# Performance work log

Measured on AMD Instinct MI355X. Metric: run time of the kernel, lower is better.

Reference implementation:

```python
import jax, jax.numpy as jnp
import numpy as np

N_NODES = 20000
N_EDGES = 640000


def graph_conv(x, src, dst, W, b, n_nodes):
    """DGL GraphConv with norm='both': D_in^{-1/2} A D_out^{-1/2} X W + b."""
    ones = jnp.ones(src.shape[0], dtype=x.dtype)
    deg_out = jnp.maximum(jax.ops.segment_sum(ones, src, num_segments=n_nodes), 1.0)
    deg_in = jnp.maximum(jax.ops.segment_sum(ones, dst, num_segments=n_nodes), 1.0)
    xs = x * (deg_out ** -0.5)[:, None]          # scale src features
    agg = jax.ops.segment_sum(xs[src], dst, num_segments=n_nodes)  # [N, d]
    agg = agg * (deg_in ** -0.5)[:, None]
    return agg @ W + b


def setup_inputs() -> dict:
    key = jax.random.key(0)
    ks = jax.random.split(key, 10)
    d = 256
    scale = 1.0 / np.sqrt(d)
    return {
        "x": jax.random.normal(ks[0], (N_NODES, d), dtype=jnp.float32),
        "side_src": jax.random.randint(ks[1], (N_EDGES,), 0, N_NODES),
        "side_dst": jax.random.randint(ks[2], (N_EDGES,), 0, N_NODES),
        "upd_src": jax.random.randint(ks[3], (N_EDGES,), 0, N_NODES),
        "upd_dst": jax.random.randint(ks[4], (N_EDGES,), 0, N_NODES),
        "W1_side": jax.random.normal(ks[5], (d, d), dtype=jnp.float32) * scale,
        "b1_side": jnp.zeros((d,), dtype=jnp.float32),
        "W1_upd": jax.random.normal(ks[6], (d, d), dtype=jnp.float32) * scale,
        "b1_upd": jnp.zeros((d,), dtype=jnp.float32),
        "W2_side": jax.random.normal(ks[7], (d, d), dtype=jnp.float32) * scale,
        "b2_side": jnp.zeros((d,), dtype=jnp.float32),
        "W2_upd": jax.random.normal(ks[8], (d, d), dtype=jnp.float32) * scale,
        "b2_upd": jnp.zeros((d,), dtype=jnp.float32),
    }


def reference(x, side_src, side_dst, upd_src, upd_dst,
              W1_side, b1_side, W1_upd, b1_upd,
              W2_side, b2_side, W2_upd, b2_upd):
    n = x.shape[0]
    # layer 1: HeteroGraphConv with aggregate='sum' over relations, then relu
    h = (graph_conv(x, side_src, side_dst, W1_side, b1_side, n)
         + graph_conv(x, upd_src, upd_dst, W1_upd, b1_upd, n))
    h = jax.nn.relu(h)
    # layer 2
    out = (graph_conv(h, side_src, side_dst, W2_side, b2_side, n)
           + graph_conv(h, upd_src, upd_dst, W2_upd, b2_upd, n))
    return out
```

## Files before the change

### kernel.cpp

```cpp
#include <hip/hip_runtime.h>

typedef __attribute__((ext_vector_type(8))) short short8;
typedef __attribute__((ext_vector_type(4))) float f32x4;

#define SCHUNK 2048
#define MAXN   20480
#define NSLICE 8
#define NPB    80

__device__ inline unsigned short f2bf(float v) {
    unsigned u = __float_as_uint(v);
    u += 0x7FFFu + ((u >> 16) & 1u);
    return (unsigned short)(u >> 16);
}
__device__ inline float bf2f(unsigned short h) {
    return __uint_as_float((unsigned)h << 16);
}

__global__ void bias_sum_kernel(const float* __restrict__ b1s, const float* __restrict__ b1u,
                                const float* __restrict__ b2s, const float* __restrict__ b2u,
                                float* __restrict__ bsum1, float* __restrict__ bsum2) {
    int i = threadIdx.x;
    bsum1[i] = b1s[i] + b1u[i];
    bsum2[i] = b2s[i] + b2u[i];
}

__global__ void wprep_kernel(const float* __restrict__ W1s, const float* __restrict__ W1u,
                             const float* __restrict__ W2s, const float* __restrict__ W2u,
                             unsigned short* __restrict__ Bpk1, unsigned short* __restrict__ Bpk2) {
    int k = blockIdx.x;
    int nn = threadIdx.x;
    int layer = blockIdx.y;
    const float* Ws = layer ? W2s : W1s;
    const float* Wu = layer ? W2u : W1u;
    float w = (k < 256) ? Ws[k * 256 + nn] : Wu[(k - 256) * 256 + nn];
    unsigned short hi = f2bf(w);
    unsigned short lo = f2bf(w - bf2f(hi));
    unsigned short* B = layer ? Bpk2 : Bpk1;
    size_t frag = ((size_t)(nn >> 4) * 16 + (k >> 5)) * 2;
    size_t addr = frag * 512 + ((nn & 15) + ((k >> 3) & 3) * 16) * 8 + (k & 7);
    B[addr] = hi;
    B[addr + 512] = lo;
}

__global__ __launch_bounds__(256) void hist_kernel(
    const int* __restrict__ sS, const int* __restrict__ dS,
    const int* __restrict__ sU, const int* __restrict__ dU,
    int Es, int Eu, int n, int nblk, unsigned int* __restrict__ histG) {
    __shared__ unsigned int h[MAXN];
    const int rel = blockIdx.y;
    const int* src = rel ? sU : sS;
    const int* dst = rel ? dU : dS;
    int E = rel ? Eu : Es;
    int b = blockIdx.x;
    int chunk = (E + nblk - 1) / nblk;
    int beg = b * chunk;
    int end = min(E, beg + chunk);
    for (int i = threadIdx.x; i < n; i += 256) h[i] = 0u;
    __syncthreads();
    for (int i = beg + threadIdx.x; i < end; i += 256) {
        atomicAdd(&h[src[i]], 1u);
        atomicAdd(&h[dst[i]], 0x10000u);
    }
    __syncthreads();
    unsigned int* out = histG + ((size_t)rel * nblk + b) * n;
    for (int i = threadIdx.x; i < n; i += 256) out[i] = h[i];
}

__global__ void totals_kernel(const unsigned int* __restrict__ histG, int n, int nblk,
                              float* __restrict__ sOutS, float* __restrict__ sInS,
                              float* __restrict__ sOutU, float* __restrict__ sInU,
                              int* __restrict__ degInS, int* __restrict__ degInU) {
    const int rel = blockIdx.y;
    int i = blockIdx.x * 256 + threadIdx.x;
    if (i >= n) return;
    const unsigned int* hg = histG + (size_t)rel * nblk * n;
    unsigned int lo = 0, hi = 0;
    for (int b = 0; b < nblk; ++b) {
        unsigned int v = hg[(size_t)b * n + i];
        lo += v & 0xFFFFu;
        hi += v >> 16;
    }
    float so = rsqrtf((float)(lo > 1u ? lo : 1u));
    float si = rsqrtf((float)(hi > 1u ? hi : 1u));
    if (rel) { sOutU[i] = so; sInU[i] = si; degInU[i] = (int)hi; }
    else     { sOutS[i] = so; sInS[i] = si; degInS[i] = (int)hi; }
}

__global__ __launch_bounds__(256) void scan_part_kernel(const int* __restrict__ degA,
                                                        const int* __restrict__ degB,
                                                        int n, int NB, int* __restrict__ bsum) {
    const int rel = blockIdx.y;
    const int* deg = rel ? degB : degA;
    int t = threadIdx.x;
    int base = blockIdx.x * SCHUNK + t * 8;
    int s = 0;
    if (base + 8 <= n) {
        int4 a = *(const int4*)(deg + base);
        int4 b = *(const int4*)(deg + base + 4);
        s = a.x + a.y + a.z + a.w + b.x + b.y + b.z + b.w;
    } else {
        for (int i = 0; i < 8; ++i)
            if (base + i < n) s += deg[base + i];
    }
    __shared__ int sm[256];
    sm[t] = s;
    __syncthreads();
    for (int off = 128; off > 0; off >>= 1) {
        if (t < off) sm[t] += sm[t + off];
        __syncthreads();
    }
    if (t == 0) bsum[rel * NB + blockIdx.x] = sm[0];
}

__global__ void scan_mid_kernel(int* __restrict__ bsum, int NB,
                                int* __restrict__ rpA, int* __restrict__ rpB, int n) {
    int t = threadIdx.x;
    if (t >= 2) return;
    int* bs = bsum + t * NB;
    int run = 0;
    for (int i = 0; i < NB; ++i) {
        int v = bs[i];
        bs[i] = run;
        run += v;
    }
    int* rp = t ? rpB : rpA;
    rp[n] = run;
}

__global__ __launch_bounds__(256) void scan_final_kernel(const int* __restrict__ degA,
                                                         const int* __restrict__ degB,
                                                         const int* __restrict__ bsum,
                                                         int n, int NB,
                                                         int* __restrict__ rpA,
                                                         int* __restrict__ rpB) {
    const int rel = blockIdx.y;
    const int* deg = rel ? degB : degA;
    int* rp = rel ? rpB : rpA;
    int t = threadIdx.x;
    int base = blockIdx.x * SCHUNK + t * 8;
    int v[8];
    if (base + 8 <= n) {
        int4 a = *(const int4*)(deg + base);
        int4 b = *(const int4*)(deg + base + 4);
        v[0] = a.x; v[1] = a.y; v[2] = a.z; v[3] = a.w;
        v[4] = b.x; v[5] = b.y; v[6] = b.z; v[7] = b.w;
    } else {
        for (int i = 0; i < 8; ++i) v[i] = (base + i < n) ? deg[base + i] : 0;
    }
    int s = 0;
    #pragma unroll
    for (int i = 0; i < 8; ++i) s += v[i];
    __shared__ int sm[256];
    sm[t] = s;
    __syncthreads();
    #pragma unroll
    for (int off = 1; off < 256; off <<= 1) {
        int y = (t >= off) ? sm[t - off] : 0;
        __syncthreads();
        sm[t] += y;
        __syncthreads();
    }
    int run = bsum[rel * NB + blockIdx.x] + sm[t] - s;
    #pragma unroll
    for (int i = 0; i < 8; ++i) {
        if (base + i < n) rp[base + i] = run;
        run += v[i];
    }
}

__global__ void offsets_kernel(const unsigned int* __restrict__ histG,
                               const int* __restrict__ rpS, const int* __restrict__ rpU,
                               int n, int nblk, int* __restrict__ offsG) {
    const int rel = blockIdx.y;
    int i = blockIdx.x * 256 + threadIdx.x;
    if (i >= n) return;
    const unsigned int* hg = histG + (size_t)rel * nblk * n;
    int* og = offsG + (size_t)rel * nblk * n;
    int run = (rel ? rpU : rpS)[i];
    for (int b = 0; b < nblk; ++b) {
        og[(size_t)b * n + i] = run;
        run += (int)(hg[(size_t)b * n + i] >> 16);
    }
}

__global__ __launch_bounds__(256) void csr_scatter_kernel(
    const int* __restrict__ sS, const int* __restrict__ dS,
    const int* __restrict__ sU, const int* __restrict__ dU,
    int Es, int Eu, int n, int nblk, const int* __restrict__ offsG,
    const float* __restrict__ sOutS, const float* __restrict__ sOutU,
    int2* __restrict__ csrPS, int2* __restrict__ csrPU) {
    __shared__ int off[MAXN];
    const int rel = blockIdx.y;
    const int* src = rel ? sU : sS;
    const int* dst = rel ? dU : dS;
    const float* so = rel ? sOutU : sOutS;
    int2* csrP = rel ? csrPU : csrPS;
    int E = rel ? Eu : Es;
    int b = blockIdx.x;
    int chunk = (E + nblk - 1) / nblk;
    int beg = b * chunk;
    int end = min(E, beg + chunk);
    const int* og = offsG + ((size_t)rel * nblk + b) * n;
    for (int i = threadIdx.x; i < n; i += 256) off[i] = og[i];
    __syncthreads();
    for (int i = beg + threadIdx.x; i < end; i += 256) {
        int s = src[i];
        int pos = atomicAdd(&off[dst[i]], 1);
        csrP[pos] = make_int2(s, __float_as_int(so[s]));
    }
}

__global__ __launch_bounds__(256) void pull_slice_kernel(
    const float4* __restrict__ xin,
    const int2* __restrict__ csrPS, const int2* __restrict__ csrPU,
    const int* __restrict__ rpS, const int* __restrict__ rpU,
    const float* __restrict__ sinS, const float* __restrict__ sinU,
    unsigned short* __restrict__ aggPk, int n) {
    int bid = blockIdx.x;
    int slice = bid & (NSLICE - 1);
    int rest = bid >> 3;
    int rel = rest & 1;
    int chunk = rest >> 1;
    const int2* csrP = rel ? csrPU : csrPS;
    const int* rp = rel ? rpU : rpS;
    const float* sinv = rel ? sinU : sinS;

    int wave = threadIdx.x >> 6;
    int lane = threadIdx.x & 63;
    int sub = lane >> 3;
    int sl = lane & 7;
    int fbase = slice * 8 + sl;

    int start = chunk * NPB;
    int lim = min(n, start + NPB);
    for (int node = start + wave; node < lim; node += 4) {
        int beg = rp[node], end = rp[node + 1];
        float ax = 0.f, ay = 0.f, az = 0.f, aw = 0.f;
        for (int eb = beg; eb < end; eb += 64) {
            int cnt = end - eb;
            if (cnt > 64) cnt = 64;
            int myu = 0;
            float myw = 0.f;
            if (lane < cnt) {
                int2 p = csrP[eb + lane];
                myu = p.x;
                myw = __int_as_float(p.y);
            }
            int jmax = (cnt + 7) >> 3;
            int j = 0;
            for (; j + 4 <= jmax; j += 4) {
                int i0 = j * 8 + sub;
                int u0 = __shfl(myu, i0);
                int u1 = __shfl(myu, i0 + 8);
                int u2 = __shfl(myu, i0 + 16);
                int u3 = __shfl(myu, i0 + 24);
                float w0 = __shfl(myw, i0);
                float w1 = __shfl(myw, i0 + 8);
                float w2 = __shfl(myw, i0 + 16);
                float w3 = __shfl(myw, i0 + 24);
                float4 a0 = xin[(size_t)u0 * 64 + fbase];
                float4 a1 = xin[(size_t)u1 * 64 + fbase];
                float4 a2 = xin[(size_t)u2 * 64 + fbase];
                float4 a3 = xin[(size_t)u3 * 64 + fbase];
                ax += w0 * a0.x + w1 * a1.x + w2 * a2.x + w3 * a3.x;
                ay += w0 * a0.y + w1 * a1.y + w2 * a2.y + w3 * a3.y;
                az += w0 * a0.z + w1 * a1.z + w2 * a2.z + w3 * a3.z;
                aw += w0 * a0.w + w1 * a1.w + w2 * a2.w + w3 * a3.w;
            }
            for (; j < jmax; ++j) {
                int idx = j * 8 + sub;
                int u = __shfl(myu, idx);
                float w = __shfl(myw, idx);
                float4 a = xin[(size_t)u * 64 + fbase];
                ax += w * a.x; ay += w * a.y; az += w * a.z; aw += w * a.w;
            }
        }
        ax += __shfl_xor(ax, 8);  ax += __shfl_xor(ax, 16); ax += __shfl_xor(ax, 32);
        ay += __shfl_xor(ay, 8);  ay += __shfl_xor(ay, 16); ay += __shfl_xor(ay, 32);
        az += __shfl_xor(az, 8);  az += __shfl_xor(az, 16); az += __shfl_xor(az, 32);
        aw += __shfl_xor(aw, 8);  aw += __shfl_xor(aw, 16); aw += __shfl_xor(aw, 32);
        if (sub == 0) {
            float si = sinv[node];
            float vx = si * ax, vy = si * ay, vz = si * az, vw = si * aw;
            ushort4 hi4 = make_ushort4(f2bf(vx), f2bf(vy), f2bf(vz), f2bf(vw));
            ushort4 lo4 = make_ushort4(f2bf(vx - bf2f(hi4.x)), f2bf(vy - bf2f(hi4.y)),
                                       f2bf(vz - bf2f(hi4.z)), f2bf(vw - bf2f(hi4.w)));
            int kstepg = rel * 8 + slice;
            size_t frag = ((size_t)(node >> 4) * 16 + kstepg) * 2;
            size_t addr = frag * 512 + ((node & 15) + (sl >> 1) * 16) * 8 + (sl & 1) * 4;
            *(ushort4*)&aggPk[addr] = hi4;
            *(ushort4*)&aggPk[addr + 512] = lo4;
        }
    }
}

#define GLOAD(AH, AL, BH, BL, KS) {                                          \
    _Pragma("unroll")                                                        \
    for (int fr = 0; fr < 2; ++fr) {                                         \
        size_t fa = ((size_t)(mt0 + fr) * 16 + (KS)) * 128 + lane;           \
        AH[fr] = Apk[fa];                                                    \
        AL[fr] = Apk[fa + 64];                                               \
    }                                                                        \
    _Pragma("unroll")                                                        \
    for (int fc = 0; fc < 4; ++fc) {                                         \
        size_t fb = ((size_t)(nt0 + fc) * 16 + (KS)) * 128 + lane;           \
        BH[fc] = Bpk[fb];                                                    \
        BL[fc] = Bpk[fb + 64];                                               \
    }                                                                        \
}

#define GMFMA(AH, AL, BH, BL) {                                              \
    _Pragma("unroll")                                                        \
    for (int fr = 0; fr < 2; ++fr)                                           \
    _Pragma("unroll")                                                        \
    for (int fc = 0; fc < 4; ++fc) {                                         \
        acc[fr][fc] = __builtin_amdgcn_mfma_f32_16x16x32_bf16(AH[fr], BH[fc], acc[fr][fc], 0, 0, 0); \
        acc[fr][fc] = __builtin_amdgcn_mfma_f32_16x16x32_bf16(AL[fr], BH[fc], acc[fr][fc], 0, 0, 0); \
        acc[fr][fc] = __builtin_amdgcn_mfma_f32_16x16x32_bf16(AH[fr], BL[fc], acc[fr][fc], 0, 0, 0); \
    }                                                                        \
}

template <int RELU>
__global__ __launch_bounds__(256) void gemm_mfma_kernel(
    const short8* __restrict__ Apk, const short8* __restrict__ Bpk,
    const float* __restrict__ bias, float* __restrict__ C, int M) {
    int lane = threadIdx.x & 63;
    int wv = threadIdx.x >> 6;
    int m0 = blockIdx.x * 32;
    if (m0 >= M) return;
    int mt0 = blockIdx.x * 2;
    int nt0 = wv * 4;
    int col0 = wv * 64;
    int frow = lane & 15;

    f32x4 acc[2][4];
    #pragma unroll
    for (int fr = 0; fr < 2; ++fr)
        #pragma unroll
        for (int fc = 0; fc < 4; ++fc)
            acc[fr][fc] = (f32x4){0.f, 0.f, 0.f, 0.f};

    short8 ahA[2], alA[2], bhA[4], blA[4];
    short8 ahB[2], alB[2], bhB[4], blB[4];
    GLOAD(ahA, alA, bhA, blA, 0);
    #pragma unroll
    for (int kp = 0; kp < 8; ++kp) {
        GLOAD(ahB, alB, bhB, blB, 2 * kp + 1);
        GMFMA(ahA, alA, bhA, blA);
        if (kp < 7) GLOAD(ahA, alA, bhA, blA, 2 * kp + 2);
        GMFMA(ahB, alB, bhB, blB);
    }

    #pragma unroll
    for (int fr = 0; fr < 2; ++fr)
        #pragma unroll
        for (int fc = 0; fc < 4; ++fc) {
            int c = col0 + fc * 16 + frow;
            float bc = bias[c];
            int rb = m0 + fr * 16 + (lane >> 4) * 4;
            #pragma unroll
            for (int j = 0; j < 4; ++j) {
                int r = rb + j;
                if (r < M) {
                    float v = acc[fr][fc][j] + bc;
                    if (RELU) v = fmaxf(v, 0.f);
                    C[(size_t)r * 256 + c] = v;
                }
            }
        }
}

extern "C" void kernel_launch(void* const* d_in, const int* in_sizes, int n_in,
                              void* d_out, int out_size, void* d_ws, size_t ws_size,
                              hipStream_t stream) {
    const float* x   = (const float*)d_in[0];
    const int* sS    = (const int*)d_in[1];
    const int* dS    = (const int*)d_in[2];
    const int* sU    = (const int*)d_in[3];
    const int* dU    = (const int*)d_in[4];
    const float* W1s = (const float*)d_in[5];
    const float* b1s = (const float*)d_in[6];
    const float* W1u = (const float*)d_in[7];
    const float* b1u = (const float*)d_in[8];
    const float* W2s = (const float*)d_in[9];
    const float* b2s = (const float*)d_in[10];
    const float* W2u = (const float*)d_in[11];
    const float* b2u = (const float*)d_in[12];
    float* out = (float*)d_out;

    const int n  = in_sizes[0] / 256;
    const int Es = in_sizes[1];
    const int Eu = in_sizes[3];
    const int NB = (n + SCHUNK - 1) / SCHUNK;
    const int mtiles = (n + 15) / 16;
    const size_t BPK_BYTES = (size_t)16 * 16 * 2 * 512 * 2;

    auto plan = [&](int nb) -> size_t {
        size_t t = 0;
        auto add = [&](size_t b) { t = (t + 255) & ~(size_t)255; t += b; };
        add((size_t)2 * nb * n * 4);
        add((size_t)2 * nb * n * 4);
        add((size_t)(n + 1) * 4); add((size_t)(n + 1) * 4);
        add((size_t)n * 4); add((size_t)n * 4); add((size_t)n * 4); add((size_t)n * 4);
        add((size_t)n * 4); add((size_t)n * 4);
        add(256 * 4); add(256 * 4);
        add((size_t)2 * NB * 4);
        add((size_t)Es * 8); add((size_t)Eu * 8);
        add(2 * BPK_BYTES);
        add((size_t)mtiles * 16 * 2 * 512 * 2);
        add((size_t)n * 256 * 4);
        return t;
    };
    const int nblk = (plan(128) <= ws_size) ? 128 : 32;

    char* ws = (char*)d_ws;
    size_t off = 0;
    auto alloc = [&](size_t bytes) -> void* {
        off = (off + 255) & ~(size_t)255;
        void* p = ws + off;
        off += bytes;
        return p;
    };

    unsigned int* histG = (unsigned int*)alloc((size_t)2 * nblk * n * 4);
    int* offsG   = (int*)alloc((size_t)2 * nblk * n * 4);
    int* rpS     = (int*)alloc((size_t)(n + 1) * 4);
    int* rpU     = (int*)alloc((size_t)(n + 1) * 4);
    float* sOutS = (float*)alloc((size_t)n * 4);
    float* sInS  = (float*)alloc((size_t)n * 4);
    float* sOutU = (float*)alloc((size_t)n * 4);
    float* sInU  = (float*)alloc((size_t)n * 4);
    int* degInS  = (int*)alloc((size_t)n * 4);
    int* degInU  = (int*)alloc((size_t)n * 4);
    float* bsum1 = (float*)alloc(256 * 4);
    float* bsum2 = (float*)alloc(256 * 4);
    int* bsumBlk = (int*)alloc((size_t)2 * NB * 4);
    int2* csrPS  = (int2*)alloc((size_t)Es * 8);
    int2* csrPU  = (int2*)alloc((size_t)Eu * 8);
    unsigned short* Bpk1 = (unsigned short*)alloc(2 * BPK_BYTES);
    unsigned short* Bpk2 = Bpk1 + BPK_BYTES / 2;
    unsigned short* aggPk = (unsigned short*)alloc((size_t)mtiles * 16 * 2 * 512 * 2);
    float* h     = (float*)alloc((size_t)n * 256 * 4);

    bias_sum_kernel<<<1, 256, 0, stream>>>(b1s, b1u, b2s, b2u, bsum1, bsum2);
    wprep_kernel<<<dim3(512, 2), 256, 0, stream>>>(W1s, W1u, W2s, W2u, Bpk1, Bpk2);
    dim3 hg(nblk, 2);
    hist_kernel<<<hg, 256, 0, stream>>>(sS, dS, sU, dU, Es, Eu, n, nblk, histG);
    dim3 tg((n + 255) / 256, 2);
    totals_kernel<<<tg, 256, 0, stream>>>(histG, n, nblk, sOutS, sInS, sOutU, sInU,
                                          degInS, degInU);
    dim3 sg(NB, 2);
    scan_part_kernel<<<sg, 256, 0, stream>>>(degInS, degInU, n, NB, bsumBlk);
    scan_mid_kernel<<<1, 64, 0, stream>>>(bsumBlk, NB, rpS, rpU, n);
    scan_final_kernel<<<sg, 256, 0, stream>>>(degInS, degInU, bsumBlk, n, NB, rpS, rpU);
    offsets_kernel<<<tg, 256, 0, stream>>>(histG, rpS, rpU, n, nblk, offsG);
    csr_scatter_kernel<<<hg, 256, 0, stream>>>(sS, dS, sU, dU, Es, Eu, n, nblk, offsG,
                                               sOutS, sOutU, csrPS, csrPU);

    int chunks = (n + NPB - 1) / NPB;
    int pullGrid = NSLICE * 2 * chunks;
    int gemmGrid = (n + 31) / 32;
    const float4* x4 = (const float4*)x;
    const float4* h4 = (const float4*)h;
    const short8* A8 = (const short8*)aggPk;
    const short8* B81 = (const short8*)Bpk1;
    const short8* B82 = (const short8*)Bpk2;

    pull_slice_kernel<<<pullGrid, 256, 0, stream>>>(x4, csrPS, csrPU, rpS, rpU,
                                                    sInS, sInU, aggPk, n);
    gemm_mfma_kernel<1><<<gemmGrid, 256, 0, stream>>>(A8, B81, bsum1, h, n);
    pull_slice_kernel<<<pullGrid, 256, 0, stream>>>(h4, csrPS, csrPU, rpS, rpU,
                                                    sInS, sInU, aggPk, n);
    gemm_mfma_kernel<0><<<gemmGrid, 256, 0, stream>>>(A8, B82, bsum2, out, n);
}
```

Baseline: 487.7 us.

## Degree-sort nodes so each 8-lane group pulls its own node, retile GEMM

Adds a counting-sort kernel that orders destination nodes by in-degree. The pull kernel now assigns one node to each 8-lane subgroup instead of one node per wave, and sorting balances trip counts so neighboring subgroups do similar work. This removes the cross-lane reductions and the idle lanes on low-degree nodes. The GEMM is retiled to 80-row blocks with 512 threads and loses its double-buffered loads, and NPB changes to 64. The extra sort kernel runs on only two blocks, and because nodes are permuted, aggPk writes are scattered.

```diff
diff --git a/kernel.cpp b/kernel.cpp
--- a/kernel.cpp
+++ b/kernel.cpp
@@ -6,7 +6,7 @@
 #define SCHUNK 2048
 #define MAXN   20480
 #define NSLICE 8
-#define NPB    80
+#define NPB    64
 
 __device__ inline unsigned short f2bf(float v) {
     unsigned u = __float_as_uint(v);
@@ -87,6 +87,40 @@
     else     { sOutS[i] = so; sInS[i] = si; degInS[i] = (int)hi; }
 }
 
+__global__ __launch_bounds__(256) void sortperm_kernel(
+    const int* __restrict__ degInS, const int* __restrict__ degInU,
+    int n, int* __restrict__ permS, int* __restrict__ permU) {
+    const int rel = blockIdx.x;
+    const int* deg = rel ? degInU : degInS;
+    int* perm = rel ? permU : permS;
+    __shared__ unsigned cnt[256];
+    __shared__ unsigned scan[256];
+    int t = threadIdx.x;
+    cnt[t] = 0;
+    __syncthreads();
+    for (int i = t; i < n; i += 256) {
+        int b = deg[i]; b = b > 255 ? 255 : b;
+        atomicAdd(&cnt[b], 1u);
+    }
+    __syncthreads();
+    unsigned v = cnt[t];
+    scan[t] = v;
+    __syncthreads();
+    for (int off = 1; off < 256; off <<= 1) {
+        unsigned y = (t >= off) ? scan[t - off] : 0u;
+        __syncthreads();
+        scan[t] += y;
+        __syncthreads();
+    }
+    cnt[t] = scan[t] - v;
+    __syncthreads();
+    for (int i = t; i < n; i += 256) {
+        int b = deg[i]; b = b > 255 ? 255 : b;
+        unsigned pos = atomicAdd(&cnt[b], 1u);
+        perm[pos] = i;
+    }
+}
+
 __global__ __launch_bounds__(256) void scan_part_kernel(const int* __restrict__ degA,
                                                         const int* __restrict__ degB,
                                                         int n, int NB, int* __restrict__ bsum) {
@@ -216,6 +250,7 @@
     const int2* __restrict__ csrPS, const int2* __restrict__ csrPU,
     const int* __restrict__ rpS, const int* __restrict__ rpU,
     const float* __restrict__ sinS, const float* __restrict__ sinU,
+    const int* __restrict__ permS, const int* __restrict__ permU,
     unsigned short* __restrict__ aggPk, int n) {
     int bid = blockIdx.x;
     int slice = bid & (NSLICE - 1);
@@ -225,68 +260,45 @@
     const int2* csrP = rel ? csrPU : csrPS;
     const int* rp = rel ? rpU : rpS;
     const float* sinv = rel ? sinU : sinS;
+    const int* perm = rel ? permU : permS;
 
     int wave = threadIdx.x >> 6;
     int lane = threadIdx.x & 63;
     int sub = lane >> 3;
     int sl = lane & 7;
     int fbase = slice * 8 + sl;
+    int subbase = lane & 56;
+    int kstepg = rel * 8 + slice;
 
     int start = chunk * NPB;
     int lim = min(n, start + NPB);
-    for (int node = start + wave; node < lim; node += 4) {
-        int beg = rp[node], end = rp[node + 1];
+    for (int nb = start + wave * 8; nb < lim; nb += 32) {
+        int pidx = nb + sub;
+        bool valid = pidx < lim;
+        int node = valid ? perm[pidx] : 0;
+        int beg = 0, end = 0;
+        if (valid) { beg = rp[node]; end = rp[node + 1]; }
         float ax = 0.f, ay = 0.f, az = 0.f, aw = 0.f;
-        for (int eb = beg; eb < end; eb += 64) {
-            int cnt = end - eb;
-            if (cnt > 64) cnt = 64;
-            int myu = 0;
-            float myw = 0.f;
-            if (lane < cnt) {
-                int2 p = csrP[eb + lane];
-                myu = p.x;
-                myw = __int_as_float(p.y);
-            }
-            int jmax = (cnt + 7) >> 3;
-            int j = 0;
-            for (; j + 4 <= jmax; j += 4) {
-                int i0 = j * 8 + sub;
-                int u0 = __shfl(myu, i0);
-                int u1 = __shfl(myu, i0 + 8);
-                int u2 = __shfl(myu, i0 + 16);
-                int u3 = __shfl(myu, i0 + 24);
-                float w0 = __shfl(myw, i0);
-                float w1 = __shfl(myw, i0 + 8);
-                float w2 = __shfl(myw, i0 + 16);
-                float w3 = __shfl(myw, i0 + 24);
-                float4 a0 = xin[(size_t)u0 * 64 + fbase];
-                float4 a1 = xin[(size_t)u1 * 64 + fbase];
-                float4 a2 = xin[(size_t)u2 * 64 + fbase];
-                float4 a3 = xin[(size_t)u3 * 64 + fbase];
-                ax += w0 * a0.x + w1 * a1.x + w2 * a2.x + w3 * a3.x;
-                ay += w0 * a0.y + w1 * a1.y + w2 * a2.y + w3 * a3.y;
-                az += w0 * a0.z + w1 * a1.z + w2 * a2.z + w3 * a3.z;
-                aw += w0 * a0.w + w1 * a1.w + w2 * a2.w + w3 * a3.w;
-            }
-            for (; j < jmax; ++j) {
-                int idx = j * 8 + sub;
-                int u = __shfl(myu, idx);
-                float w = __shfl(myw, idx);
+        int eb = beg;
+        while (__any(eb < end)) {
+            int ei = eb + sl;
+            int2 p = make_int2(0, 0);
+            if (ei < end) p = csrP[ei];
+            #pragma unroll
+            for (int j = 0; j < 8; ++j) {
+                int u = __shfl(p.x, subbase | j);
+                float w = __int_as_float(__shfl(p.y, subbase | j));
                 float4 a = xin[(size_t)u * 64 + fbase];
                 ax += w * a.x; ay += w * a.y; az += w * a.z; aw += w * a.w;
             }
+            eb += 8;
         }
-        ax += __shfl_xor(ax, 8);  ax += __shfl_xor(ax, 16); ax += __shfl_xor(ax, 32);
-        ay += __shfl_xor(ay, 8);  ay += __shfl_xor(ay, 16); ay += __shfl_xor(ay, 32);
-        az += __shfl_xor(az, 8);  az += __shfl_xor(az, 16); az += __shfl_xor(az, 32);
-        aw += __shfl_xor(aw, 8);  aw += __shfl_xor(aw, 16); aw += __shfl_xor(aw, 32);
-        if (sub == 0) {
+        if (valid) {
             float si = sinv[node];
             float vx = si * ax, vy = si * ay, vz = si * az, vw = si * aw;
             ushort4 hi4 = make_ushort4(f2bf(vx), f2bf(vy), f2bf(vz), f2bf(vw));
             ushort4 lo4 = make_ushort4(f2bf(vx - bf2f(hi4.x)), f2bf(vy - bf2f(hi4.y)),
                                        f2bf(vz - bf2f(hi4.z)), f2bf(vw - bf2f(hi4.w)));
-            int kstepg = rel * 8 + slice;
             size_t frag = ((size_t)(node >> 4) * 16 + kstepg) * 2;
             size_t addr = frag * 512 + ((node & 15) + (sl >> 1) * 16) * 8 + (sl & 1) * 4;
             *(ushort4*)&aggPk[addr] = hi4;
@@ -295,67 +307,55 @@
     }
 }
 
-#define GLOAD(AH, AL, BH, BL, KS) {                                          \
-    _Pragma("unroll")                                                        \
-    for (int fr = 0; fr < 2; ++fr) {                                         \
-        size_t fa = ((size_t)(mt0 + fr) * 16 + (KS)) * 128 + lane;           \
-        AH[fr] = Apk[fa];                                                    \
-        AL[fr] = Apk[fa + 64];                                               \
-    }                                                                        \
-    _Pragma("unroll")                                                        \
-    for (int fc = 0; fc < 4; ++fc) {                                         \
-        size_t fb = ((size_t)(nt0 + fc) * 16 + (KS)) * 128 + lane;           \
-        BH[fc] = Bpk[fb];                                                    \
-        BL[fc] = Bpk[fb + 64];                                               \
-    }                                                                        \
-}
-
-#define GMFMA(AH, AL, BH, BL) {                                              \
-    _Pragma("unroll")                                                        \
-    for (int fr = 0; fr < 2; ++fr)                                           \
-    _Pragma("unroll")                                                        \
-    for (int fc = 0; fc < 4; ++fc) {                                         \
-        acc[fr][fc] = __builtin_amdgcn_mfma_f32_16x16x32_bf16(AH[fr], BH[fc], acc[fr][fc], 0, 0, 0); \
-        acc[fr][fc] = __builtin_amdgcn_mfma_f32_16x16x32_bf16(AL[fr], BH[fc], acc[fr][fc], 0, 0, 0); \
-        acc[fr][fc] = __builtin_amdgcn_mfma_f32_16x16x32_bf16(AH[fr], BL[fc], acc[fr][fc], 0, 0, 0); \
-    }                                                                        \
-}
-
 template <int RELU>
-__global__ __launch_bounds__(256) void gemm_mfma_kernel(
+__global__ __launch_bounds__(512) void gemm_mfma_kernel(
     const short8* __restrict__ Apk, const short8* __restrict__ Bpk,
     const float* __restrict__ bias, float* __restrict__ C, int M) {
     int lane = threadIdx.x & 63;
     int wv = threadIdx.x >> 6;
-    int m0 = blockIdx.x * 32;
+    int mt0 = blockIdx.x * 5;
+    int m0 = blockIdx.x * 80;
     if (m0 >= M) return;
-    int mt0 = blockIdx.x * 2;
-    int nt0 = wv * 4;
-    int col0 = wv * 64;
+    int nt0 = wv * 2;
+    int col0 = wv * 32;
     int frow = lane & 15;
 
-    f32x4 acc[2][4];
-    #pragma unroll
-    for (int fr = 0; fr < 2; ++fr)
+    f32x4 acc[5][2];
+    #pragma unroll
+    for (int fr = 0; fr < 5; ++fr)
         #pragma unroll
-        for (int fc = 0; fc < 4; ++fc)
+        for (int fc = 0; fc < 2; ++fc)
             acc[fr][fc] = (f32x4){0.f, 0.f, 0.f, 0.f};
 
-    short8 ahA[2], alA[2], bhA[4], blA[4];
-    short8 ahB[2], alB[2], bhB[4], blB[4];
-    GLOAD(ahA, alA, bhA, blA, 0);
-    #pragma unroll
-    for (int kp = 0; kp < 8; ++kp) {
-        GLOAD(ahB, alB, bhB, blB, 2 * kp + 1);
-        GMFMA(ahA, alA, bhA, blA);
-        if (kp < 7) GLOAD(ahA, alA, bhA, blA, 2 * kp + 2);
-        GMFMA(ahB, alB, bhB, blB);
-    }
-
-    #pragma unroll
-    for (int fr = 0; fr < 2; ++fr)
+    #pragma unroll
+    for (int ks = 0; ks < 16; ++ks) {
+        short8 ah[5], al[5], bh[2], bl[2];
         #pragma unroll
-        for (int fc = 0; fc < 4; ++fc) {
+        for (int fr = 0; fr < 5; ++fr) {
+            size_t fa = ((size_t)(mt0 + fr) * 16 + ks) * 128 + lane;
+            ah[fr] = Apk[fa];
+            al[fr] = Apk[fa + 64];
+        }
+        #pragma unroll
+        for (int fc = 0; fc < 2; ++fc) {
+            size_t fb = ((size_t)(nt0 + fc) * 16 + ks) * 128 + lane;
+            bh[fc] = Bpk[fb];
+            bl[fc] = Bpk[fb + 64];
+        }
+        #pragma unroll
+        for (int fr = 0; fr < 5; ++fr)
+            #pragma unroll
+            for (int fc = 0; fc < 2; ++fc) {
+                acc[fr][fc] = __builtin_amdgcn_mfma_f32_16x16x32_bf16(ah[fr], bh[fc], acc[fr][fc], 0, 0, 0);
+                acc[fr][fc] = __builtin_amdgcn_mfma_f32_16x16x32_bf16(al[fr], bh[fc], acc[fr][fc], 0, 0, 0);
+                acc[fr][fc] = __builtin_amdgcn_mfma_f32_16x16x32_bf16(ah[fr], bl[fc], acc[fr][fc], 0, 0, 0);
+            }
+    }
+
+    #pragma unroll
+    for (int fr = 0; fr < 5; ++fr)
+        #pragma unroll
+        for (int fc = 0; fc < 2; ++fc) {
             int c = col0 + fc * 16 + frow;
             float bc = bias[c];
             int rb = m0 + fr * 16 + (lane >> 4) * 4;
@@ -393,7 +393,8 @@
     const int Es = in_sizes[1];
     const int Eu = in_sizes[3];
     const int NB = (n + SCHUNK - 1) / SCHUNK;
-    const int mtiles = (n + 15) / 16;
+    const int gemmGrid = (n + 79) / 80;
+    const size_t AGG_BYTES = (size_t)gemmGrid * 5 * 16 * 2 * 512 * 2;
     const size_t BPK_BYTES = (size_t)16 * 16 * 2 * 512 * 2;
 
     auto plan = [&](int nb) -> size_t {
@@ -404,11 +405,12 @@
         add((size_t)(n + 1) * 4); add((size_t)(n + 1) * 4);
         add((size_t)n * 4); add((size_t)n * 4); add((size_t)n * 4); add((size_t)n * 4);
         add((size_t)n * 4); add((size_t)n * 4);
+        add((size_t)n * 4); add((size_t)n * 4);
         add(256 * 4); add(256 * 4);
         add((size_t)2 * NB * 4);
         add((size_t)Es * 8); add((size_t)Eu * 8);
         add(2 * BPK_BYTES);
-        add((size_t)mtiles * 16 * 2 * 512 * 2);
+        add(AGG_BYTES);
         add((size_t)n * 256 * 4);
         return t;
     };
@@ -433,6 +435,8 @@
     float* sInU  = (float*)alloc((size_t)n * 4);
     int* degInS  = (int*)alloc((size_t)n * 4);
     int* degInU  = (int*)alloc((size_t)n * 4);
+    int* permS   = (int*)alloc((size_t)n * 4);
+    int* permU   = (int*)alloc((size_t)n * 4);
     float* bsum1 = (float*)alloc(256 * 4);
     float* bsum2 = (float*)alloc(256 * 4);
     int* bsumBlk = (int*)alloc((size_t)2 * NB * 4);
@@ -440,7 +444,7 @@
     int2* csrPU  = (int2*)alloc((size_t)Eu * 8);
     unsigned short* Bpk1 = (unsigned short*)alloc(2 * BPK_BYTES);
     unsigned short* Bpk2 = Bpk1 + BPK_BYTES / 2;
-    unsigned short* aggPk = (unsigned short*)alloc((size_t)mtiles * 16 * 2 * 512 * 2);
+    unsigned short* aggPk = (unsigned short*)alloc(AGG_BYTES);
     float* h     = (float*)alloc((size_t)n * 256 * 4);
 
     bias_sum_kernel<<<1, 256, 0, stream>>>(b1s, b1u, b2s, b2u, bsum1, bsum2);
@@ -450,6 +454,7 @@
     dim3 tg((n + 255) / 256, 2);
     totals_kernel<<<tg, 256, 0, stream>>>(histG, n, nblk, sOutS, sInS, sOutU, sInU,
                                           degInS, degInU);
+    sortperm_kernel<<<2, 256, 0, stream>>>(degInS, degInU, n, permS, permU);
     dim3 sg(NB, 2);
     scan_part_kernel<<<sg, 256, 0, stream>>>(degInS, degInU, n, NB, bsumBlk);
     scan_mid_kernel<<<1, 64, 0, stream>>>(bsumBlk, NB, rpS, rpU, n);
@@ -460,7 +465,6 @@
 
     int chunks = (n + NPB - 1) / NPB;
     int pullGrid = NSLICE * 2 * chunks;
-    int gemmGrid = (n + 31) / 32;
     const float4* x4 = (const float4*)x;
     const float4* h4 = (const float4*)h;
     const short8* A8 = (const short8*)aggPk;
@@ -468,9 +472,9 @@
     const short8* B82 = (const short8*)Bpk2;
 
     pull_slice_kernel<<<pullGrid, 256, 0, stream>>>(x4, csrPS, csrPU, rpS, rpU,
-                                                    sInS, sInU, aggPk, n);
-    gemm_mfma_kernel<1><<<gemmGrid, 256, 0, stream>>>(A8, B81, bsum1, h, n);
+                                                    sInS, sInU, permS, permU, aggPk, n);
+    gemm_mfma_kernel<1><<<gemmGrid, 512, 0, stream>>>(A8, B81, bsum1, h, n);
     pull_slice_kernel<<<pullGrid, 256, 0, stream>>>(h4, csrPS, csrPU, rpS, rpU,
-                                                    sInS, sInU, aggPk, n);
-    gemm_mfma_kernel<0><<<gemmGrid, 256, 0, stream>>>(A8, B82, bsum2, out, n);
-}
+                                                    sInS, sInU, permS, permU, aggPk, n);
+    gemm_mfma_kernel<0><<<gemmGrid, 512, 0, stream>>>(A8, B82, bsum2, out, n);
+}
```

New measurement: 550.7 us. 12.9% more time.

## Retile MFMA GEMM to 80-row blocks with 8 waves and halve pull chunk

Applied to the files above, without the earlier changes.

The GEMM now uses 512-thread blocks. Each block covers 80 rows (5 m-tiles) and each wave covers 32 columns, replacing 32-row blocks of 4 waves with 64 columns each. The explicit double-buffered register prefetch is dropped in favour of a simple per-k-step load then MFMA loop. The aggregate buffer is padded to a multiple of 80 rows, and the pull kernel's nodes per block drop from 80 to 40 to launch more blocks. The aim is more reuse of each loaded A fragment across waves and better parallelism, at the risk of exposed load latency without the prefetch and a different occupancy profile.

```diff
diff --git a/kernel.cpp b/kernel.cpp
--- a/kernel.cpp
+++ b/kernel.cpp
@@ -6,7 +6,7 @@
 #define SCHUNK 2048
 #define MAXN   20480
 #define NSLICE 8
-#define NPB    80
+#define NPB    40
 
 __device__ inline unsigned short f2bf(float v) {
     unsigned u = __float_as_uint(v);
@@ -231,6 +231,7 @@
     int sub = lane >> 3;
     int sl = lane & 7;
     int fbase = slice * 8 + sl;
+    int kstepg = rel * 8 + slice;
 
     int start = chunk * NPB;
     int lim = min(n, start + NPB);
@@ -286,7 +287,6 @@
             ushort4 hi4 = make_ushort4(f2bf(vx), f2bf(vy), f2bf(vz), f2bf(vw));
             ushort4 lo4 = make_ushort4(f2bf(vx - bf2f(hi4.x)), f2bf(vy - bf2f(hi4.y)),
                                        f2bf(vz - bf2f(hi4.z)), f2bf(vw - bf2f(hi4.w)));
-            int kstepg = rel * 8 + slice;
             size_t frag = ((size_t)(node >> 4) * 16 + kstepg) * 2;
             size_t addr = frag * 512 + ((node & 15) + (sl >> 1) * 16) * 8 + (sl & 1) * 4;
             *(ushort4*)&aggPk[addr] = hi4;
@@ -295,67 +295,55 @@
     }
 }
 
-#define GLOAD(AH, AL, BH, BL, KS) {                                          \
-    _Pragma("unroll")                                                        \
-    for (int fr = 0; fr < 2; ++fr) {                                         \
-        size_t fa = ((size_t)(mt0 + fr) * 16 + (KS)) * 128 + lane;           \
-        AH[fr] = Apk[fa];                                                    \
-        AL[fr] = Apk[fa + 64];                                               \
-    }                                                                        \
-    _Pragma("unroll")                                                        \
-    for (int fc = 0; fc < 4; ++fc) {                                         \
-        size_t fb = ((size_t)(nt0 + fc) * 16 + (KS)) * 128 + lane;           \
-        BH[fc] = Bpk[fb];                                                    \
-        BL[fc] = Bpk[fb + 64];                                               \
-    }                                                                        \
-}
-
-#define GMFMA(AH, AL, BH, BL) {                                              \
-    _Pragma("unroll")                                                        \
-    for (int fr = 0; fr < 2; ++fr)                                           \
-    _Pragma("unroll")                                                        \
-    for (int fc = 0; fc < 4; ++fc) {                                         \
-        acc[fr][fc] = __builtin_amdgcn_mfma_f32_16x16x32_bf16(AH[fr], BH[fc], acc[fr][fc], 0, 0, 0); \
-        acc[fr][fc] = __builtin_amdgcn_mfma_f32_16x16x32_bf16(AL[fr], BH[fc], acc[fr][fc], 0, 0, 0); \
-        acc[fr][fc] = __builtin_amdgcn_mfma_f32_16x16x32_bf16(AH[fr], BL[fc], acc[fr][fc], 0, 0, 0); \
-    }                                                                        \
-}
-
 template <int RELU>
-__global__ __launch_bounds__(256) void gemm_mfma_kernel(
+__global__ __launch_bounds__(512) void gemm_mfma_kernel(
     const short8* __restrict__ Apk, const short8* __restrict__ Bpk,
     const float* __restrict__ bias, float* __restrict__ C, int M) {
     int lane = threadIdx.x & 63;
     int wv = threadIdx.x >> 6;
-    int m0 = blockIdx.x * 32;
+    int mt0 = blockIdx.x * 5;
+    int m0 = blockIdx.x * 80;
     if (m0 >= M) return;
-    int mt0 = blockIdx.x * 2;
-    int nt0 = wv * 4;
-    int col0 = wv * 64;
+    int nt0 = wv * 2;
+    int col0 = wv * 32;
     int frow = lane & 15;
 
-    f32x4 acc[2][4];
-    #pragma unroll
-    for (int fr = 0; fr < 2; ++fr)
+    f32x4 acc[5][2];
+    #pragma unroll
+    for (int fr = 0; fr < 5; ++fr)
         #pragma unroll
-        for (int fc = 0; fc < 4; ++fc)
+        for (int fc = 0; fc < 2; ++fc)
             acc[fr][fc] = (f32x4){0.f, 0.f, 0.f, 0.f};
 
-    short8 ahA[2], alA[2], bhA[4], blA[4];
-    short8 ahB[2], alB[2], bhB[4], blB[4];
-    GLOAD(ahA, alA, bhA, blA, 0);
-    #pragma unroll
-    for (int kp = 0; kp < 8; ++kp) {
-        GLOAD(ahB, alB, bhB, blB, 2 * kp + 1);
-        GMFMA(ahA, alA, bhA, blA);
-        if (kp < 7) GLOAD(ahA, alA, bhA, blA, 2 * kp + 2);
-        GMFMA(ahB, alB, bhB, blB);
-    }
-
-    #pragma unroll
-    for (int fr = 0; fr < 2; ++fr)
+    #pragma unroll
+    for (int ks = 0; ks < 16; ++ks) {
+        short8 ah[5], al[5], bh[2], bl[2];
         #pragma unroll
-        for (int fc = 0; fc < 4; ++fc) {
+        for (int fr = 0; fr < 5; ++fr) {
+            size_t fa = ((size_t)(mt0 + fr) * 16 + ks) * 128 + lane;
+            ah[fr] = Apk[fa];
+            al[fr] = Apk[fa + 64];
+        }
+        #pragma unroll
+        for (int fc = 0; fc < 2; ++fc) {
+            size_t fb = ((size_t)(nt0 + fc) * 16 + ks) * 128 + lane;
+            bh[fc] = Bpk[fb];
+            bl[fc] = Bpk[fb + 64];
+        }
+        #pragma unroll
+        for (int fr = 0; fr < 5; ++fr)
+            #pragma unroll
+            for (int fc = 0; fc < 2; ++fc) {
+                acc[fr][fc] = __builtin_amdgcn_mfma_f32_16x16x32_bf16(ah[fr], bh[fc], acc[fr][fc], 0, 0, 0);
+                acc[fr][fc] = __builtin_amdgcn_mfma_f32_16x16x32_bf16(al[fr], bh[fc], acc[fr][fc], 0, 0, 0);
+                acc[fr][fc] = __builtin_amdgcn_mfma_f32_16x16x32_bf16(ah[fr], bl[fc], acc[fr][fc], 0, 0, 0);
+            }
+    }
+
+    #pragma unroll
+    for (int fr = 0; fr < 5; ++fr)
+        #pragma unroll
+        for (int fc = 0; fc < 2; ++fc) {
             int c = col0 + fc * 16 + frow;
             float bc = bias[c];
             int rb = m0 + fr * 16 + (lane >> 4) * 4;
@@ -393,7 +381,8 @@
     const int Es = in_sizes[1];
     const int Eu = in_sizes[3];
     const int NB = (n + SCHUNK - 1) / SCHUNK;
-    const int mtiles = (n + 15) / 16;
+    const int gemmGrid = (n + 79) / 80;
+    const size_t AGG_BYTES = (size_t)gemmGrid * 5 * 16 * 2 * 512 * 2;
     const size_t BPK_BYTES = (size_t)16 * 16 * 2 * 512 * 2;
 
     auto plan = [&](int nb) -> size_t {
@@ -408,7 +397,7 @@
         add((size_t)2 * NB * 4);
         add((size_t)Es * 8); add((size_t)Eu * 8);
         add(2 * BPK_BYTES);
-        add((size_t)mtiles * 16 * 2 * 512 * 2);
+        add(AGG_BYTES);
         add((size_t)n * 256 * 4);
         return t;
     };
@@ -440,7 +429,7 @@
     int2* csrPU  = (int2*)alloc((size_t)Eu * 8);
     unsigned short* Bpk1 = (unsigned short*)alloc(2 * BPK_BYTES);
     unsigned short* Bpk2 = Bpk1 + BPK_BYTES / 2;
-    unsigned short* aggPk = (unsigned short*)alloc((size_t)mtiles * 16 * 2 * 512 * 2);
+    unsigned short* aggPk = (unsigned short*)alloc(AGG_BYTES);
     float* h     = (float*)alloc((size_t)n * 256 * 4);
 
     bias_sum_kernel<<<1, 256, 0, stream>>>(b1s, b1u, b2s, b2u, bsum1, bsum2);
@@ -460,7 +449,6 @@
 
     int chunks = (n + NPB - 1) / NPB;
     int pullGrid = NSLICE * 2 * chunks;
-    int gemmGrid = (n + 31) / 32;
     const float4* x4 = (const float4*)x;
     const float4* h4 = (const float4*)h;
     const short8* A8 = (const short8*)aggPk;
@@ -469,8 +457,8 @@
 
     pull_slice_kernel<<<pullGrid, 256, 0, stream>>>(x4, csrPS, csrPU, rpS, rpU,
                                                     sInS, sInU, aggPk, n);
-    gemm_mfma_kernel<1><<<gemmGrid, 256, 0, stream>>>(A8, B81, bsum1, h, n);
+    gemm_mfma_kernel<1><<<gemmGrid, 512, 0, stream>>>(A8, B81, bsum1, h, n);
     pull_slice_kernel<<<pullGrid, 256, 0, stream>>>(h4, csrPS, csrPU, rpS, rpU,
                                                     sInS, sInU, aggPk, n);
-    gemm_mfma_kernel<0><<<gemmGrid, 256, 0, stream>>>(A8, B82, bsum2, out, n);
-}
+    gemm_mfma_kernel<0><<<gemmGrid, 512, 0, stream>>>(A8, B82, bsum2, out, n);
+}
```

Result: no change. 484.2 us (-0.7%).
